# Performance work log

Measured on AMD Instinct MI355X. Metric: run time of the kernel, lower is better.

The kernel has to match this reference:

```python
import jax, jax.numpy as jnp
import numpy as np

BAG = 15          # bag_size
STEPS = 5
LAM = 1e-3        # anti_hebb_lambda
PS = 8            # patch_size
IM = 28           # image_size
DEN = IM - PS     # position normalization denominator (=20)
KEEP = 0.1        # 1 - recurrent_sparsity


def _ln(h, gamma, beta, eps=1e-5):
    mu = jnp.mean(h, axis=-1, keepdims=True)
    var = jnp.mean((h - mu) ** 2, axis=-1, keepdims=True)
    return (h - mu) * jax.lax.rsqrt(var + eps) * gamma + beta


def _patch(img, pos):
    # img: [IM, IM], pos: [2] int32 -> flattened PSxPS patch [PS*PS]
    return jax.lax.dynamic_slice(img, (pos[0], pos[1]), (PS, PS)).reshape(PS * PS)

_extract = jax.vmap(_patch)  # [B,IM,IM], [B,2] -> [B, PS*PS]


def setup_inputs() -> dict:
    key = jax.random.key(0)
    ks = jax.random.split(key, 8)
    B = 65536
    x = jax.random.normal(ks[0], (B, 1, IM, IM), jnp.float32)
    in_dim = PS * PS + 2
    Wi = jax.random.normal(ks[1], (BAG, in_dim), jnp.float32) * np.sqrt(2.0 / in_dim)
    bi = jnp.zeros((BAG,), jnp.float32)
    gamma = jnp.ones((BAG,), jnp.float32)
    beta = jnp.zeros((BAG,), jnp.float32)
    mask = (jax.random.uniform(ks[2], (BAG, BAG)) < KEEP).astype(jnp.float32)
    R = jax.random.normal(ks[3], (BAG, BAG), jnp.float32) * np.sqrt(2.0 / BAG) * mask
    rb = jnp.zeros((BAG,), jnp.float32)
    Wc = jax.random.normal(ks[4], (2, BAG), jnp.float32) * np.sqrt(2.0 / BAG)
    bc = jnp.zeros((2,), jnp.float32)
    Wo = jax.random.normal(ks[5], (10, BAG), jnp.float32) * np.sqrt(2.0 / BAG)
    bo = jnp.zeros((10,), jnp.float32)
    return dict(x=x, Wi=Wi, bi=bi, gamma=gamma, beta=beta, R=R, rb=rb,
                mask=mask, Wc=Wc, bc=bc, Wo=Wo, bo=bo)


def reference(x, Wi, bi, gamma, beta, R, rb, mask, Wc, bc, Wo, bo):
    B = x.shape[0]
    imgs = x[:, 0]  # [B, IM, IM]
    positions = jnp.full((B, 2), (IM - PS) // 2, dtype=jnp.int32)
    state = None
    logits = None
    for _ in range(STEPS):  # small fixed step count; state/positions recur
        flat = _extract(imgs, positions)                       # [B, 64]
        pos = positions.astype(x.dtype) / DEN * 2.0 - 1.0      # [B, 2]
        in_act = jnp.concatenate([flat, pos], axis=1) @ Wi.T + bi
        if state is None:
            state = _ln(jax.nn.relu(in_act), gamma, beta)
        else:
            coact = jnp.einsum('bi,bj->ij', state, state) / B  # [BAG, BAG]
            Reff = (R - LAM * coact) * mask
            state = _ln(jax.nn.relu(in_act + state @ Reff.T + rb), gamma, beta)
        logits = state @ Wo.T + bo                             # [B, 10]
        ctrl = jnp.tanh(state @ Wc.T + bc)                     # [B, 2]
        mag_r = jnp.abs(ctrl[:, 0])
        mag_c = jnp.abs(ctrl[:, 1])
        row_sel = mag_r >= mag_c
        row_move = jnp.where(row_sel, jnp.sign(ctrl[:, 0]).astype(jnp.int32), 0)
        col_move = jnp.where(row_sel, 0, jnp.sign(ctrl[:, 1]).astype(jnp.int32))
        positions = jnp.clip(positions + jnp.stack([row_move, col_move], axis=1), 0, IM - PS)
    return logits
```

## Files before the change

kernel.cpp:

```cpp
#include <hip/hip_runtime.h>
#include <math.h>

#define BAGN 15
#define PSZ 8
#define IMSZ 28
#define LAMF 0.001f

template<bool FIRST, bool LAST>
__global__ __launch_bounds__(256) void step_kernel(
    const float* __restrict__ x,
    const float* __restrict__ Wi, const float* __restrict__ bi,
    const float* __restrict__ gamma, const float* __restrict__ beta,
    const float* __restrict__ R, const float* __restrict__ rb,
    const float* __restrict__ mask,
    const float* __restrict__ Wc, const float* __restrict__ bc,
    const float* __restrict__ Wo, const float* __restrict__ bo,
    float* __restrict__ state_io, int* __restrict__ pos_io,
    const float* __restrict__ coact_in, float* __restrict__ coact_out,
    float* __restrict__ out, int B, float invB)
{
    __shared__ float sWi[15 * 72];
    __shared__ float sBi[15], sGa[15], sBe[15], sRb[15];
    __shared__ float sWc[30], sBc[2], sWo[150], sBo[10];
    __shared__ float sReff[225];
    __shared__ float sS[256 * 16];

    const int tid = threadIdx.x;

    for (int idx = tid; idx < 990; idx += 256) {
        int u = idx / 66, k = idx - u * 66;
        sWi[u * 72 + k] = Wi[idx];
    }
    if (tid < 15) {
        sBi[tid] = bi[tid]; sGa[tid] = gamma[tid];
        sBe[tid] = beta[tid]; sRb[tid] = rb[tid];
    }
    if (tid >= 32 && tid < 62) sWc[tid - 32] = Wc[tid - 32];
    if (tid >= 64 && tid < 66) sBc[tid - 64] = bc[tid - 64];
    if (LAST) {
        if (tid >= 96 && tid < 246) sWo[tid - 96] = Wo[tid - 96];
        if (tid >= 246 && tid < 256) sBo[tid - 246] = bo[tid - 246];
    }
    if (!FIRST) {
        if (tid < 225)
            sReff[tid] = (R[tid] - LAMF * (coact_in[tid] * invB)) * mask[tid];
    }
    __syncthreads();

    const int b = blockIdx.x * 256 + tid;

    int pr, pc;
    if (FIRST) { pr = 10; pc = 10; }
    else { pr = pos_io[b]; pc = pos_io[B + b]; }

    const float* img = x + (size_t)b * (IMSZ * IMSZ);
    float patch[64];
#pragma unroll
    for (int r = 0; r < 8; ++r) {
        const float* rowp = img + (pr + r) * IMSZ + pc;
#pragma unroll
        for (int c = 0; c < 8; ++c) patch[r * 8 + c] = rowp[c];
    }
    const float posr = ((float)pr / 20.0f) * 2.0f - 1.0f;
    const float posc = ((float)pc / 20.0f) * 2.0f - 1.0f;

    float sprev[15];
    if (!FIRST) {
#pragma unroll
        for (int j = 0; j < 15; ++j) sprev[j] = state_io[j * B + b];
    }

    float h[15];
#pragma unroll
    for (int u = 0; u < 15; ++u) {
        const float* w = sWi + u * 72;
        float a = 0.0f;
#pragma unroll
        for (int k = 0; k < 64; ++k) a = fmaf(patch[k], w[k], a);
        a = fmaf(posr, w[64], a);
        a = fmaf(posc, w[65], a);
        a += sBi[u];
        if (!FIRST) {
            float r2 = 0.0f;
#pragma unroll
            for (int j = 0; j < 15; ++j) r2 = fmaf(sprev[j], sReff[u * 15 + j], r2);
            a += r2 + sRb[u];
        }
        h[u] = a > 0.0f ? a : 0.0f;
    }

    float mu = 0.0f;
#pragma unroll
    for (int u = 0; u < 15; ++u) mu += h[u];
    mu *= (1.0f / 15.0f);
    float var = 0.0f;
#pragma unroll
    for (int u = 0; u < 15; ++u) { float d = h[u] - mu; var = fmaf(d, d, var); }
    var *= (1.0f / 15.0f);
    const float rs = 1.0f / sqrtf(var + 1e-5f);
    float s[15];
#pragma unroll
    for (int u = 0; u < 15; ++u) s[u] = (h[u] - mu) * rs * sGa[u] + sBe[u];

    if (LAST) {
#pragma unroll
        for (int o = 0; o < 10; ++o) {
            float a = 0.0f;
#pragma unroll
            for (int j = 0; j < 15; ++j) a = fmaf(s[j], sWo[o * 15 + j], a);
            out[(size_t)b * 10 + o] = a + sBo[o];
        }
    } else {
#pragma unroll
        for (int j = 0; j < 15; ++j) state_io[j * B + b] = s[j];

        float c0 = 0.0f, c1 = 0.0f;
#pragma unroll
        for (int j = 0; j < 15; ++j) {
            c0 = fmaf(s[j], sWc[j], c0);
            c1 = fmaf(s[j], sWc[15 + j], c1);
        }
        c0 = tanhf(c0 + sBc[0]);
        c1 = tanhf(c1 + sBc[1]);
        const float m0 = fabsf(c0), m1 = fabsf(c1);
        int rm, cm;
        if (m0 >= m1) { rm = (c0 > 0.0f) - (c0 < 0.0f); cm = 0; }
        else          { rm = 0; cm = (c1 > 0.0f) - (c1 < 0.0f); }
        pr += rm; pc += cm;
        pr = min(max(pr, 0), IMSZ - PSZ);
        pc = min(max(pc, 0), IMSZ - PSZ);
        pos_io[b] = pr;
        pos_io[B + b] = pc;

#pragma unroll
        for (int j = 0; j < 15; ++j) sS[tid * 16 + j] = s[j];
        __syncthreads();
        if (tid < 225) {
            int i = tid / 15, j = tid - i * 15;
            float acc = 0.0f;
#pragma unroll 8
            for (int bb = 0; bb < 256; ++bb)
                acc = fmaf(sS[bb * 16 + i], sS[bb * 16 + j], acc);
            atomicAdd(&coact_out[tid], acc);
        }
    }
}

extern "C" void kernel_launch(void* const* d_in, const int* in_sizes, int n_in,
                              void* d_out, int out_size, void* d_ws, size_t ws_size,
                              hipStream_t stream) {
    const float* x     = (const float*)d_in[0];
    const float* Wi    = (const float*)d_in[1];
    const float* bi    = (const float*)d_in[2];
    const float* gamma = (const float*)d_in[3];
    const float* beta  = (const float*)d_in[4];
    const float* R     = (const float*)d_in[5];
    const float* rb    = (const float*)d_in[6];
    const float* mask  = (const float*)d_in[7];
    const float* Wc    = (const float*)d_in[8];
    const float* bc    = (const float*)d_in[9];
    const float* Wo    = (const float*)d_in[10];
    const float* bo    = (const float*)d_in[11];
    float* out = (float*)d_out;

    const int B = in_sizes[0] / (IMSZ * IMSZ);
    const int grid = B / 256;
    const float invB = 1.0f / (float)B;

    float* wsf = (float*)d_ws;
    float* state = wsf;
    int* pos = (int*)(wsf + (size_t)B * 15);
    float* coact = wsf + (size_t)B * 15 + (size_t)B * 2;

    hipMemsetAsync(coact, 0, 4 * 256 * sizeof(float), stream);

    step_kernel<true, false><<<grid, 256, 0, stream>>>(
        x, Wi, bi, gamma, beta, R, rb, mask, Wc, bc, Wo, bo,
        state, pos, nullptr, coact, nullptr, B, invB);
    step_kernel<false, false><<<grid, 256, 0, stream>>>(
        x, Wi, bi, gamma, beta, R, rb, mask, Wc, bc, Wo, bo,
        state, pos, coact, coact + 256, nullptr, B, invB);
    step_kernel<false, false><<<grid, 256, 0, stream>>>(
        x, Wi, bi, gamma, beta, R, rb, mask, Wc, bc, Wo, bo,
        state, pos, coact + 256, coact + 512, nullptr, B, invB);
    step_kernel<false, false><<<grid, 256, 0, stream>>>(
        x, Wi, bi, gamma, beta, R, rb, mask, Wc, bc, Wo, bo,
        state, pos, coact + 512, coact + 768, nullptr, B, invB);
    step_kernel<false, true><<<grid, 256, 0, stream>>>(
        x, Wi, bi, gamma, beta, R, rb, mask, Wc, bc, Wo, bo,
        state, pos, coact + 768, nullptr, out, B, invB);
}
```

Baseline: 383.8 us.

## Fuse all recurrent steps into one cooperative kernel with grid-wide syncs

Replaces the five per-step launches with a single cooperative kernel that loops over the steps. Recurrent state and patch positions stay in registers instead of round-tripping through global workspace. A grid.sync after each step's coactivation reduction provides the global dependency. The coactivation accumulators are padded to a 16-float stride so concurrent atomics do not share cache lines. In exchange it pays for grid-wide barriers and requires all 256 blocks to be co-resident, which limits occupancy for hiding the latency of the patch gathers.

```diff
diff --git a/kernel.cpp b/kernel.cpp
--- a/kernel.cpp
+++ b/kernel.cpp
@@ -1,13 +1,14 @@
 #include <hip/hip_runtime.h>
+#include <hip/hip_cooperative_groups.h>
 #include <math.h>
 
-#define BAGN 15
+namespace cg = cooperative_groups;
+
+#define IMSZ 28
 #define PSZ 8
-#define IMSZ 28
 #define LAMF 0.001f
 
-template<bool FIRST, bool LAST>
-__global__ __launch_bounds__(256) void step_kernel(
+__global__ __launch_bounds__(256) void cyclic_fused(
     const float* __restrict__ x,
     const float* __restrict__ Wi, const float* __restrict__ bi,
     const float* __restrict__ gamma, const float* __restrict__ beta,
@@ -15,14 +16,15 @@
     const float* __restrict__ mask,
     const float* __restrict__ Wc, const float* __restrict__ bc,
     const float* __restrict__ Wo, const float* __restrict__ bo,
-    float* __restrict__ state_io, int* __restrict__ pos_io,
-    const float* __restrict__ coact_in, float* __restrict__ coact_out,
+    float* __restrict__ coact,
     float* __restrict__ out, int B, float invB)
 {
+    cg::grid_group grid = cg::this_grid();
+
     __shared__ float sWi[15 * 72];
-    __shared__ float sBi[15], sGa[15], sBe[15], sRb[15];
-    __shared__ float sWc[30], sBc[2], sWo[150], sBo[10];
-    __shared__ float sReff[225];
+    __shared__ float sBi[16], sGa[16], sBe[16], sRb[16];
+    __shared__ float sWc[32], sBc[2], sWo[160], sBo[16];
+    __shared__ float sR[240], sM[240], sReff[240];
     __shared__ float sS[256 * 16];
 
     const int tid = threadIdx.x;
@@ -31,117 +33,110 @@
         int u = idx / 66, k = idx - u * 66;
         sWi[u * 72 + k] = Wi[idx];
     }
+    if (tid < 225) { sR[tid] = R[tid]; sM[tid] = mask[tid]; }
     if (tid < 15) {
         sBi[tid] = bi[tid]; sGa[tid] = gamma[tid];
         sBe[tid] = beta[tid]; sRb[tid] = rb[tid];
     }
-    if (tid >= 32 && tid < 62) sWc[tid - 32] = Wc[tid - 32];
-    if (tid >= 64 && tid < 66) sBc[tid - 64] = bc[tid - 64];
-    if (LAST) {
-        if (tid >= 96 && tid < 246) sWo[tid - 96] = Wo[tid - 96];
-        if (tid >= 246 && tid < 256) sBo[tid - 246] = bo[tid - 246];
-    }
-    if (!FIRST) {
-        if (tid < 225)
-            sReff[tid] = (R[tid] - LAMF * (coact_in[tid] * invB)) * mask[tid];
-    }
+    if (tid < 30)  sWc[tid] = Wc[tid];
+    if (tid < 2)   sBc[tid] = bc[tid];
+    if (tid < 150) sWo[tid] = Wo[tid];
+    if (tid < 10)  sBo[tid] = bo[tid];
     __syncthreads();
 
     const int b = blockIdx.x * 256 + tid;
+    const float* img = x + (size_t)b * (IMSZ * IMSZ);
 
-    int pr, pc;
-    if (FIRST) { pr = 10; pc = 10; }
-    else { pr = pos_io[b]; pc = pos_io[B + b]; }
+    int pr = 10, pc = 10;
+    float st[15];
 
-    const float* img = x + (size_t)b * (IMSZ * IMSZ);
-    float patch[64];
+    for (int s = 0; s < 5; ++s) {
+        float patch[64];
 #pragma unroll
-    for (int r = 0; r < 8; ++r) {
-        const float* rowp = img + (pr + r) * IMSZ + pc;
+        for (int r = 0; r < 8; ++r) {
+            const float* rowp = img + (pr + r) * IMSZ + pc;
 #pragma unroll
-        for (int c = 0; c < 8; ++c) patch[r * 8 + c] = rowp[c];
-    }
-    const float posr = ((float)pr / 20.0f) * 2.0f - 1.0f;
-    const float posc = ((float)pc / 20.0f) * 2.0f - 1.0f;
+            for (int c = 0; c < 8; ++c) patch[r * 8 + c] = rowp[c];
+        }
+        const float posr = ((float)pr / 20.0f) * 2.0f - 1.0f;
+        const float posc = ((float)pc / 20.0f) * 2.0f - 1.0f;
 
-    float sprev[15];
-    if (!FIRST) {
+        float h[15];
 #pragma unroll
-        for (int j = 0; j < 15; ++j) sprev[j] = state_io[j * B + b];
-    }
-
-    float h[15];
-#pragma unroll
-    for (int u = 0; u < 15; ++u) {
-        const float* w = sWi + u * 72;
-        float a = 0.0f;
-#pragma unroll
-        for (int k = 0; k < 64; ++k) a = fmaf(patch[k], w[k], a);
-        a = fmaf(posr, w[64], a);
-        a = fmaf(posc, w[65], a);
-        a += sBi[u];
-        if (!FIRST) {
-            float r2 = 0.0f;
-#pragma unroll
-            for (int j = 0; j < 15; ++j) r2 = fmaf(sprev[j], sReff[u * 15 + j], r2);
-            a += r2 + sRb[u];
-        }
-        h[u] = a > 0.0f ? a : 0.0f;
-    }
-
-    float mu = 0.0f;
-#pragma unroll
-    for (int u = 0; u < 15; ++u) mu += h[u];
-    mu *= (1.0f / 15.0f);
-    float var = 0.0f;
-#pragma unroll
-    for (int u = 0; u < 15; ++u) { float d = h[u] - mu; var = fmaf(d, d, var); }
-    var *= (1.0f / 15.0f);
-    const float rs = 1.0f / sqrtf(var + 1e-5f);
-    float s[15];
-#pragma unroll
-    for (int u = 0; u < 15; ++u) s[u] = (h[u] - mu) * rs * sGa[u] + sBe[u];
-
-    if (LAST) {
-#pragma unroll
-        for (int o = 0; o < 10; ++o) {
+        for (int u = 0; u < 15; ++u) {
+            const float* w = sWi + u * 72;
             float a = 0.0f;
 #pragma unroll
-            for (int j = 0; j < 15; ++j) a = fmaf(s[j], sWo[o * 15 + j], a);
-            out[(size_t)b * 10 + o] = a + sBo[o];
+            for (int k = 0; k < 64; ++k) a = fmaf(patch[k], w[k], a);
+            a = fmaf(posr, w[64], a);
+            a = fmaf(posc, w[65], a);
+            a += sBi[u];
+            if (s > 0) {
+                float r2 = 0.0f;
+#pragma unroll
+                for (int j = 0; j < 15; ++j) r2 = fmaf(st[j], sReff[u * 15 + j], r2);
+                a += r2 + sRb[u];
+            }
+            h[u] = fmaxf(a, 0.0f);
         }
-    } else {
+
+        float mu = 0.0f;
 #pragma unroll
-        for (int j = 0; j < 15; ++j) state_io[j * B + b] = s[j];
+        for (int u = 0; u < 15; ++u) mu += h[u];
+        mu *= (1.0f / 15.0f);
+        float var = 0.0f;
+#pragma unroll
+        for (int u = 0; u < 15; ++u) { float d = h[u] - mu; var = fmaf(d, d, var); }
+        var *= (1.0f / 15.0f);
+        const float rs = 1.0f / sqrtf(var + 1e-5f);
+#pragma unroll
+        for (int u = 0; u < 15; ++u) st[u] = (h[u] - mu) * rs * sGa[u] + sBe[u];
 
-        float c0 = 0.0f, c1 = 0.0f;
+        if (s == 4) {
 #pragma unroll
-        for (int j = 0; j < 15; ++j) {
-            c0 = fmaf(s[j], sWc[j], c0);
-            c1 = fmaf(s[j], sWc[15 + j], c1);
-        }
-        c0 = tanhf(c0 + sBc[0]);
-        c1 = tanhf(c1 + sBc[1]);
-        const float m0 = fabsf(c0), m1 = fabsf(c1);
-        int rm, cm;
-        if (m0 >= m1) { rm = (c0 > 0.0f) - (c0 < 0.0f); cm = 0; }
-        else          { rm = 0; cm = (c1 > 0.0f) - (c1 < 0.0f); }
-        pr += rm; pc += cm;
-        pr = min(max(pr, 0), IMSZ - PSZ);
-        pc = min(max(pc, 0), IMSZ - PSZ);
-        pos_io[b] = pr;
-        pos_io[B + b] = pc;
+            for (int o = 0; o < 10; ++o) {
+                float a = 0.0f;
+#pragma unroll
+                for (int j = 0; j < 15; ++j) a = fmaf(st[j], sWo[o * 15 + j], a);
+                out[(size_t)b * 10 + o] = a + sBo[o];
+            }
+        } else {
+#pragma unroll
+            for (int j = 0; j < 15; ++j) sS[tid * 16 + j] = st[j];
 
+            float c0 = 0.0f, c1 = 0.0f;
 #pragma unroll
-        for (int j = 0; j < 15; ++j) sS[tid * 16 + j] = s[j];
-        __syncthreads();
-        if (tid < 225) {
-            int i = tid / 15, j = tid - i * 15;
-            float acc = 0.0f;
+            for (int j = 0; j < 15; ++j) {
+                c0 = fmaf(st[j], sWc[j], c0);
+                c1 = fmaf(st[j], sWc[15 + j], c1);
+            }
+            c0 = tanhf(c0 + sBc[0]);
+            c1 = tanhf(c1 + sBc[1]);
+            const float m0 = fabsf(c0), m1 = fabsf(c1);
+            int rm, cm;
+            if (m0 >= m1) { rm = (c0 > 0.0f) - (c0 < 0.0f); cm = 0; }
+            else          { rm = 0; cm = (c1 > 0.0f) - (c1 < 0.0f); }
+            pr = min(max(pr + rm, 0), IMSZ - PSZ);
+            pc = min(max(pc + cm, 0), IMSZ - PSZ);
+
+            __syncthreads();
+            if (tid < 225) {
+                int i = tid / 15, j = tid - i * 15;
+                float acc = 0.0f;
 #pragma unroll 8
-            for (int bb = 0; bb < 256; ++bb)
-                acc = fmaf(sS[bb * 16 + i], sS[bb * 16 + j], acc);
-            atomicAdd(&coact_out[tid], acc);
+                for (int bb = 0; bb < 256; ++bb)
+                    acc = fmaf(sS[bb * 16 + i], sS[bb * 16 + j], acc);
+                atomicAdd(&coact[(size_t)(s * 225 + tid) * 16], acc);
+            }
+
+            grid.sync();
+
+            if (tid < 225) {
+                float cv = __hip_atomic_load(&coact[(size_t)(s * 225 + tid) * 16],
+                                             __ATOMIC_ACQUIRE, __HIP_MEMORY_SCOPE_AGENT);
+                sReff[tid] = (sR[tid] - LAMF * (cv * invB)) * sM[tid];
+            }
+            __syncthreads();
         }
     }
 }
@@ -163,30 +158,17 @@
     const float* bo    = (const float*)d_in[11];
     float* out = (float*)d_out;
 
-    const int B = in_sizes[0] / (IMSZ * IMSZ);
-    const int grid = B / 256;
-    const float invB = 1.0f / (float)B;
+    int B = in_sizes[0] / (IMSZ * IMSZ);
+    float invB = 1.0f / (float)B;
+    float* coact = (float*)d_ws;
 
-    float* wsf = (float*)d_ws;
-    float* state = wsf;
-    int* pos = (int*)(wsf + (size_t)B * 15);
-    float* coact = wsf + (size_t)B * 15 + (size_t)B * 2;
+    hipMemsetAsync(coact, 0, (size_t)4 * 240 * 16 * sizeof(float), stream);
 
-    hipMemsetAsync(coact, 0, 4 * 256 * sizeof(float), stream);
+    void* args[] = { (void*)&x, (void*)&Wi, (void*)&bi, (void*)&gamma, (void*)&beta,
+                     (void*)&R, (void*)&rb, (void*)&mask, (void*)&Wc, (void*)&bc,
+                     (void*)&Wo, (void*)&bo, (void*)&coact, (void*)&out,
+                     (void*)&B, (void*)&invB };
 
-    step_kernel<true, false><<<grid, 256, 0, stream>>>(
-        x, Wi, bi, gamma, beta, R, rb, mask, Wc, bc, Wo, bo,
-        state, pos, nullptr, coact, nullptr, B, invB);
-    step_kernel<false, false><<<grid, 256, 0, stream>>>(
-        x, Wi, bi, gamma, beta, R, rb, mask, Wc, bc, Wo, bo,
-        state, pos, coact, coact + 256, nullptr, B, invB);
-    step_kernel<false, false><<<grid, 256, 0, stream>>>(
-        x, Wi, bi, gamma, beta, R, rb, mask, Wc, bc, Wo, bo,
-        state, pos, coact + 256, coact + 512, nullptr, B, invB);
-    step_kernel<false, false><<<grid, 256, 0, stream>>>(
-        x, Wi, bi, gamma, beta, R, rb, mask, Wc, bc, Wo, bo,
-        state, pos, coact + 512, coact + 768, nullptr, B, invB);
-    step_kernel<false, true><<<grid, 256, 0, stream>>>(
-        x, Wi, bi, gamma, beta, R, rb, mask, Wc, bc, Wo, bo,
-        state, pos, coact + 768, nullptr, out, B, invB);
+    hipLaunchCooperativeKernel((void*)cyclic_fused, dim3(B / 256), dim3(256),
+                               args, 0, stream);
 }
```

Result: slower. 534.3 us (+39.2%).

## Split each sample across 8 lanes with shuffle reduction and replicated coact atomics

Applied to the files above, without the earlier changes.

Each sample is now handled by 8 threads: each lane loads one patch row and computes partial dot products, which are combined with xor shuffles. Before, one thread gathered a whole 64-element patch with strided loads. State moves to a row-major stride-16 layout and positions are packed into one int. Coactivation partials are spread over 8 replicated accumulators to cut atomic contention, now that blocks hold 32 samples and there are 8x more of them. The cost is redundant per-lane layer-norm, control math and weight reloads in every block.

```diff
diff --git a/kernel.cpp b/kernel.cpp
--- a/kernel.cpp
+++ b/kernel.cpp
@@ -1,13 +1,14 @@
 #include <hip/hip_runtime.h>
 #include <math.h>
 
-#define BAGN 15
-#define PSZ 8
 #define IMSZ 28
+#define PSZ  8
 #define LAMF 0.001f
+#define NREP 8
+#define CSTRIDE 240
 
 template<bool FIRST, bool LAST>
-__global__ __launch_bounds__(256) void step_kernel(
+__global__ __launch_bounds__(256, 8) void step8(
     const float* __restrict__ x,
     const float* __restrict__ Wi, const float* __restrict__ bi,
     const float* __restrict__ gamma, const float* __restrict__ beta,
@@ -15,15 +16,15 @@
     const float* __restrict__ mask,
     const float* __restrict__ Wc, const float* __restrict__ bc,
     const float* __restrict__ Wo, const float* __restrict__ bo,
-    float* __restrict__ state_io, int* __restrict__ pos_io,
+    float* __restrict__ state, int* __restrict__ pos,
     const float* __restrict__ coact_in, float* __restrict__ coact_out,
     float* __restrict__ out, int B, float invB)
 {
     __shared__ float sWi[15 * 72];
-    __shared__ float sBi[15], sGa[15], sBe[15], sRb[15];
-    __shared__ float sWc[30], sBc[2], sWo[150], sBo[10];
-    __shared__ float sReff[225];
-    __shared__ float sS[256 * 16];
+    __shared__ float sBi[16], sGa[16], sBe[16], sRb[16];
+    __shared__ float sWc[32], sBc[2], sWo[160], sBo[16];
+    __shared__ float sReff[240];
+    __shared__ float sS[32 * 16];
 
     const int tid = threadIdx.x;
 
@@ -39,54 +40,69 @@
     if (tid >= 64 && tid < 66) sBc[tid - 64] = bc[tid - 64];
     if (LAST) {
         if (tid >= 96 && tid < 246) sWo[tid - 96] = Wo[tid - 96];
-        if (tid >= 246 && tid < 256) sBo[tid - 246] = bo[tid - 246];
+        if (tid >= 246) sBo[tid - 246] = bo[tid - 246];
     }
     if (!FIRST) {
-        if (tid < 225)
-            sReff[tid] = (R[tid] - LAMF * (coact_in[tid] * invB)) * mask[tid];
+        if (tid < 225) {
+            float cv = 0.0f;
+#pragma unroll
+            for (int r = 0; r < NREP; ++r) cv += coact_in[r * CSTRIDE + tid];
+            sReff[tid] = (R[tid] - LAMF * (cv * invB)) * mask[tid];
+        } else if (tid < 240) {
+            sReff[tid] = 0.0f;
+        }
     }
     __syncthreads();
 
-    const int b = blockIdx.x * 256 + tid;
+    const int sib = tid >> 3;
+    const int row = tid & 7;
+    const int b = blockIdx.x * 32 + sib;
 
     int pr, pc;
     if (FIRST) { pr = 10; pc = 10; }
-    else { pr = pos_io[b]; pc = pos_io[B + b]; }
-
-    const float* img = x + (size_t)b * (IMSZ * IMSZ);
-    float patch[64];
-#pragma unroll
-    for (int r = 0; r < 8; ++r) {
-        const float* rowp = img + (pr + r) * IMSZ + pc;
-#pragma unroll
-        for (int c = 0; c < 8; ++c) patch[r * 8 + c] = rowp[c];
-    }
+    else { int p = pos[b]; pr = p >> 8; pc = p & 255; }
+
+    const float* rowp = x + (size_t)b * (IMSZ * IMSZ) + (pr + row) * IMSZ + pc;
+    float patch[8];
+#pragma unroll
+    for (int c = 0; c < 8; ++c) patch[c] = rowp[c];
+
     const float posr = ((float)pr / 20.0f) * 2.0f - 1.0f;
     const float posc = ((float)pc / 20.0f) * 2.0f - 1.0f;
 
-    float sprev[15];
+    float sj0 = 0.0f, sj1 = 0.0f;
     if (!FIRST) {
-#pragma unroll
-        for (int j = 0; j < 15; ++j) sprev[j] = state_io[j * B + b];
+        sj0 = state[b * 16 + row];
+        sj1 = (row < 7) ? state[b * 16 + 8 + row] : 0.0f;
     }
 
     float h[15];
 #pragma unroll
     for (int u = 0; u < 15; ++u) {
-        const float* w = sWi + u * 72;
+        const float* w = sWi + u * 72 + row * 8;
         float a = 0.0f;
 #pragma unroll
-        for (int k = 0; k < 64; ++k) a = fmaf(patch[k], w[k], a);
-        a = fmaf(posr, w[64], a);
-        a = fmaf(posc, w[65], a);
-        a += sBi[u];
+        for (int c = 0; c < 8; ++c) a = fmaf(patch[c], w[c], a);
         if (!FIRST) {
-            float r2 = 0.0f;
-#pragma unroll
-            for (int j = 0; j < 15; ++j) r2 = fmaf(sprev[j], sReff[u * 15 + j], r2);
-            a += r2 + sRb[u];
-        }
-        h[u] = a > 0.0f ? a : 0.0f;
+            a = fmaf(sj0, sReff[u * 15 + row], a);
+            a = fmaf(sj1, sReff[u * 15 + 8 + row], a);
+        }
+        if (row == 0) {
+            a = fmaf(posr, sWi[u * 72 + 64], a);
+            a = fmaf(posc, sWi[u * 72 + 65], a);
+            a += sBi[u];
+            if (!FIRST) a += sRb[u];
+        }
+        h[u] = a;
+    }
+
+#pragma unroll
+    for (int u = 0; u < 15; ++u) {
+        float v = h[u];
+        v += __shfl_xor(v, 1);
+        v += __shfl_xor(v, 2);
+        v += __shfl_xor(v, 4);
+        h[u] = fmaxf(v, 0.0f);
     }
 
     float mu = 0.0f;
@@ -98,27 +114,30 @@
     for (int u = 0; u < 15; ++u) { float d = h[u] - mu; var = fmaf(d, d, var); }
     var *= (1.0f / 15.0f);
     const float rs = 1.0f / sqrtf(var + 1e-5f);
-    float s[15];
-#pragma unroll
-    for (int u = 0; u < 15; ++u) s[u] = (h[u] - mu) * rs * sGa[u] + sBe[u];
+    float st[15];
+#pragma unroll
+    for (int u = 0; u < 15; ++u) st[u] = (h[u] - mu) * rs * sGa[u] + sBe[u];
 
     if (LAST) {
 #pragma unroll
-        for (int o = 0; o < 10; ++o) {
-            float a = 0.0f;
-#pragma unroll
-            for (int j = 0; j < 15; ++j) a = fmaf(s[j], sWo[o * 15 + j], a);
-            out[(size_t)b * 10 + o] = a + sBo[o];
+        for (int rep = 0; rep < 2; ++rep) {
+            int o = rep * 8 + row;
+            if (o < 10) {
+                float a = 0.0f;
+#pragma unroll
+                for (int j = 0; j < 15; ++j) a = fmaf(st[j], sWo[o * 15 + j], a);
+                out[(size_t)b * 10 + o] = a + sBo[o];
+            }
         }
     } else {
-#pragma unroll
-        for (int j = 0; j < 15; ++j) state_io[j * B + b] = s[j];
+        state[b * 16 + row] = st[row];
+        if (row < 7) state[b * 16 + 8 + row] = st[8 + row];
 
         float c0 = 0.0f, c1 = 0.0f;
 #pragma unroll
         for (int j = 0; j < 15; ++j) {
-            c0 = fmaf(s[j], sWc[j], c0);
-            c1 = fmaf(s[j], sWc[15 + j], c1);
+            c0 = fmaf(st[j], sWc[j], c0);
+            c1 = fmaf(st[j], sWc[15 + j], c1);
         }
         c0 = tanhf(c0 + sBc[0]);
         c1 = tanhf(c1 + sBc[1]);
@@ -126,22 +145,20 @@
         int rm, cm;
         if (m0 >= m1) { rm = (c0 > 0.0f) - (c0 < 0.0f); cm = 0; }
         else          { rm = 0; cm = (c1 > 0.0f) - (c1 < 0.0f); }
-        pr += rm; pc += cm;
-        pr = min(max(pr, 0), IMSZ - PSZ);
-        pc = min(max(pc, 0), IMSZ - PSZ);
-        pos_io[b] = pr;
-        pos_io[B + b] = pc;
-
-#pragma unroll
-        for (int j = 0; j < 15; ++j) sS[tid * 16 + j] = s[j];
+        pr = min(max(pr + rm, 0), IMSZ - PSZ);
+        pc = min(max(pc + cm, 0), IMSZ - PSZ);
+        if (row == 0) pos[b] = (pr << 8) | pc;
+
+        sS[sib * 16 + row] = st[row];
+        if (row < 7) sS[sib * 16 + 8 + row] = st[8 + row];
         __syncthreads();
         if (tid < 225) {
             int i = tid / 15, j = tid - i * 15;
             float acc = 0.0f;
-#pragma unroll 8
-            for (int bb = 0; bb < 256; ++bb)
+#pragma unroll
+            for (int bb = 0; bb < 32; ++bb)
                 acc = fmaf(sS[bb * 16 + i], sS[bb * 16 + j], acc);
-            atomicAdd(&coact_out[tid], acc);
+            atomicAdd(&coact_out[(blockIdx.x & (NREP - 1)) * CSTRIDE + tid], acc);
         }
     }
 }
@@ -164,29 +181,29 @@
     float* out = (float*)d_out;
 
     const int B = in_sizes[0] / (IMSZ * IMSZ);
-    const int grid = B / 256;
     const float invB = 1.0f / (float)B;
+    const int grid = B / 32;
 
     float* wsf = (float*)d_ws;
     float* state = wsf;
-    int* pos = (int*)(wsf + (size_t)B * 15);
-    float* coact = wsf + (size_t)B * 15 + (size_t)B * 2;
-
-    hipMemsetAsync(coact, 0, 4 * 256 * sizeof(float), stream);
-
-    step_kernel<true, false><<<grid, 256, 0, stream>>>(
-        x, Wi, bi, gamma, beta, R, rb, mask, Wc, bc, Wo, bo,
-        state, pos, nullptr, coact, nullptr, B, invB);
-    step_kernel<false, false><<<grid, 256, 0, stream>>>(
-        x, Wi, bi, gamma, beta, R, rb, mask, Wc, bc, Wo, bo,
-        state, pos, coact, coact + 256, nullptr, B, invB);
-    step_kernel<false, false><<<grid, 256, 0, stream>>>(
-        x, Wi, bi, gamma, beta, R, rb, mask, Wc, bc, Wo, bo,
-        state, pos, coact + 256, coact + 512, nullptr, B, invB);
-    step_kernel<false, false><<<grid, 256, 0, stream>>>(
-        x, Wi, bi, gamma, beta, R, rb, mask, Wc, bc, Wo, bo,
-        state, pos, coact + 512, coact + 768, nullptr, B, invB);
-    step_kernel<false, true><<<grid, 256, 0, stream>>>(
-        x, Wi, bi, gamma, beta, R, rb, mask, Wc, bc, Wo, bo,
-        state, pos, coact + 768, nullptr, out, B, invB);
+    int* pos = (int*)(wsf + (size_t)B * 16);
+    float* coact = wsf + (size_t)B * 16 + (size_t)B;
+
+    hipMemsetAsync(coact, 0, (size_t)4 * NREP * CSTRIDE * sizeof(float), stream);
+
+    step8<true, false><<<grid, 256, 0, stream>>>(
+        x, Wi, bi, gamma, beta, R, rb, mask, Wc, bc, Wo, bo,
+        state, pos, nullptr, coact + 0 * NREP * CSTRIDE, nullptr, B, invB);
+    step8<false, false><<<grid, 256, 0, stream>>>(
+        x, Wi, bi, gamma, beta, R, rb, mask, Wc, bc, Wo, bo,
+        state, pos, coact + 0 * NREP * CSTRIDE, coact + 1 * NREP * CSTRIDE, nullptr, B, invB);
+    step8<false, false><<<grid, 256, 0, stream>>>(
+        x, Wi, bi, gamma, beta, R, rb, mask, Wc, bc, Wo, bo,
+        state, pos, coact + 1 * NREP * CSTRIDE, coact + 2 * NREP * CSTRIDE, nullptr, B, invB);
+    step8<false, false><<<grid, 256, 0, stream>>>(
+        x, Wi, bi, gamma, beta, R, rb, mask, Wc, bc, Wo, bo,
+        state, pos, coact + 2 * NREP * CSTRIDE, coact + 3 * NREP * CSTRIDE, nullptr, B, invB);
+    step8<false, true><<<grid, 256, 0, stream>>>(
+        x, Wi, bi, gamma, beta, R, rb, mask, Wc, bc, Wo, bo,
+        state, pos, coact + 3 * NREP * CSTRIDE, nullptr, out, B, invB);
 }
```

Result: faster. 353.3 us (-7.9%).

## Vectorize patch loads, read weights directly, symmetric coact with replicated atomics

Applied to the files above, without the earlier changes.

Patch rows are now loaded as aligned float4 triples and shifted with selects, replacing scalar gathers. Weights are read directly from global memory (uniform scalar loads) instead of being staged in shared memory, which removes the prologue barrier. The coactivation is accumulated only for the 120 upper-triangle pairs into 8 replicated accumulators selected by block index, reducing atomic contention. Positions are packed into one int, and launch bounds request a single block per SM. The risk is extra per-thread work: every thread rebuilds Reff from global coact sums (8 replicas times 225 entries), which may cost more than it saves.

```diff
diff --git a/kernel.cpp b/kernel.cpp
--- a/kernel.cpp
+++ b/kernel.cpp
@@ -1,13 +1,15 @@
 #include <hip/hip_runtime.h>
 #include <math.h>
 
-#define BAGN 15
-#define PSZ 8
 #define IMSZ 28
+#define PSZ  8
 #define LAMF 0.001f
+#define NREP 8
+#define NPAIR 120
+#define CSTR 128
 
 template<bool FIRST, bool LAST>
-__global__ __launch_bounds__(256) void step_kernel(
+__global__ __launch_bounds__(256, 1) void step_spt(
     const float* __restrict__ x,
     const float* __restrict__ Wi, const float* __restrict__ bi,
     const float* __restrict__ gamma, const float* __restrict__ beta,
@@ -15,133 +17,149 @@
     const float* __restrict__ mask,
     const float* __restrict__ Wc, const float* __restrict__ bc,
     const float* __restrict__ Wo, const float* __restrict__ bo,
-    float* __restrict__ state_io, int* __restrict__ pos_io,
+    float* __restrict__ state, int* __restrict__ pos,
     const float* __restrict__ coact_in, float* __restrict__ coact_out,
-    float* __restrict__ out, int B, float invB)
+    float* __restrict__ out, int B, float lamB)
 {
-    __shared__ float sWi[15 * 72];
-    __shared__ float sBi[15], sGa[15], sBe[15], sRb[15];
-    __shared__ float sWc[30], sBc[2], sWo[150], sBo[10];
-    __shared__ float sReff[225];
     __shared__ float sS[256 * 16];
 
     const int tid = threadIdx.x;
-
-    for (int idx = tid; idx < 990; idx += 256) {
-        int u = idx / 66, k = idx - u * 66;
-        sWi[u * 72 + k] = Wi[idx];
-    }
-    if (tid < 15) {
-        sBi[tid] = bi[tid]; sGa[tid] = gamma[tid];
-        sBe[tid] = beta[tid]; sRb[tid] = rb[tid];
-    }
-    if (tid >= 32 && tid < 62) sWc[tid - 32] = Wc[tid - 32];
-    if (tid >= 64 && tid < 66) sBc[tid - 64] = bc[tid - 64];
-    if (LAST) {
-        if (tid >= 96 && tid < 246) sWo[tid - 96] = Wo[tid - 96];
-        if (tid >= 246 && tid < 256) sBo[tid - 246] = bo[tid - 246];
-    }
-    if (!FIRST) {
-        if (tid < 225)
-            sReff[tid] = (R[tid] - LAMF * (coact_in[tid] * invB)) * mask[tid];
-    }
-    __syncthreads();
-
     const int b = blockIdx.x * 256 + tid;
+    const float* img = x + (size_t)b * (IMSZ * IMSZ);
 
     int pr, pc;
     if (FIRST) { pr = 10; pc = 10; }
-    else { pr = pos_io[b]; pc = pos_io[B + b]; }
-
-    const float* img = x + (size_t)b * (IMSZ * IMSZ);
+    else { int p = pos[b]; pr = p >> 8; pc = p & 255; }
+
     float patch[64];
-#pragma unroll
-    for (int r = 0; r < 8; ++r) {
-        const float* rowp = img + (pr + r) * IMSZ + pc;
-#pragma unroll
-        for (int c = 0; c < 8; ++c) patch[r * 8 + c] = rowp[c];
-    }
+    {
+        const int base = pr * IMSZ + pc;
+        const int a0 = base & ~3;
+        if (FIRST) {
+#pragma unroll
+            for (int r = 0; r < 8; ++r) {
+                const float4* q = (const float4*)(img + a0 + r * IMSZ);
+                float4 q0 = q[0], q1 = q[1], q2 = q[2];
+                patch[r * 8 + 0] = q0.z; patch[r * 8 + 1] = q0.w;
+                patch[r * 8 + 2] = q1.x; patch[r * 8 + 3] = q1.y;
+                patch[r * 8 + 4] = q1.z; patch[r * 8 + 5] = q1.w;
+                patch[r * 8 + 6] = q2.x; patch[r * 8 + 7] = q2.y;
+            }
+        } else {
+            const int d = base & 3;
+            const bool s2 = (d & 2) != 0, s1 = (d & 1) != 0;
+#pragma unroll
+            for (int r = 0; r < 8; ++r) {
+                const float4* q = (const float4*)(img + a0 + r * IMSZ);
+                float4 q0 = q[0], q1 = q[1], q2 = q[2];
+                const float f[12] = { q0.x, q0.y, q0.z, q0.w,
+                                      q1.x, q1.y, q1.z, q1.w,
+                                      q2.x, q2.y, q2.z, q2.w };
+                float t[9];
+#pragma unroll
+                for (int c = 0; c < 9; ++c) t[c] = s2 ? f[c + 2] : f[c];
+#pragma unroll
+                for (int c = 0; c < 8; ++c) patch[r * 8 + c] = s1 ? t[c + 1] : t[c];
+            }
+        }
+    }
+
     const float posr = ((float)pr / 20.0f) * 2.0f - 1.0f;
     const float posc = ((float)pc / 20.0f) * 2.0f - 1.0f;
 
-    float sprev[15];
-    if (!FIRST) {
-#pragma unroll
-        for (int j = 0; j < 15; ++j) sprev[j] = state_io[j * B + b];
-    }
-
     float h[15];
 #pragma unroll
     for (int u = 0; u < 15; ++u) {
-        const float* w = sWi + u * 72;
+        const float* w = Wi + u * 66;
         float a = 0.0f;
 #pragma unroll
         for (int k = 0; k < 64; ++k) a = fmaf(patch[k], w[k], a);
         a = fmaf(posr, w[64], a);
         a = fmaf(posc, w[65], a);
-        a += sBi[u];
-        if (!FIRST) {
-            float r2 = 0.0f;
-#pragma unroll
-            for (int j = 0; j < 15; ++j) r2 = fmaf(sprev[j], sReff[u * 15 + j], r2);
-            a += r2 + sRb[u];
-        }
-        h[u] = a > 0.0f ? a : 0.0f;
-    }
-
+        h[u] = a + bi[u];
+    }
+
+    if (!FIRST) {
+        float sprev[15];
+#pragma unroll
+        for (int j = 0; j < 15; ++j) sprev[j] = state[(size_t)j * B + b];
+#pragma unroll
+        for (int j = 0; j < 15; ++j) {
+            const float sj = sprev[j];
+#pragma unroll
+            for (int u = 0; u < 15; ++u) {
+                const int i0 = u < j ? u : j;
+                const int j0 = u < j ? j : u;
+                const int sid = i0 * 15 + j0 - (i0 * (i0 + 1)) / 2;
+                float cs = 0.0f;
+#pragma unroll
+                for (int rr = 0; rr < NREP; ++rr) cs += coact_in[rr * CSTR + sid];
+                const float reff = (R[u * 15 + j] - lamB * cs) * mask[u * 15 + j];
+                h[u] = fmaf(sj, reff, h[u]);
+            }
+        }
+#pragma unroll
+        for (int u = 0; u < 15; ++u) h[u] += rb[u];
+    }
+
+#pragma unroll
+    for (int u = 0; u < 15; ++u) h[u] = fmaxf(h[u], 0.0f);
     float mu = 0.0f;
 #pragma unroll
     for (int u = 0; u < 15; ++u) mu += h[u];
     mu *= (1.0f / 15.0f);
     float var = 0.0f;
 #pragma unroll
-    for (int u = 0; u < 15; ++u) { float d = h[u] - mu; var = fmaf(d, d, var); }
+    for (int u = 0; u < 15; ++u) { float dd = h[u] - mu; var = fmaf(dd, dd, var); }
     var *= (1.0f / 15.0f);
     const float rs = 1.0f / sqrtf(var + 1e-5f);
-    float s[15];
-#pragma unroll
-    for (int u = 0; u < 15; ++u) s[u] = (h[u] - mu) * rs * sGa[u] + sBe[u];
+    float st[15];
+#pragma unroll
+    for (int u = 0; u < 15; ++u) st[u] = (h[u] - mu) * rs * gamma[u] + beta[u];
 
     if (LAST) {
 #pragma unroll
         for (int o = 0; o < 10; ++o) {
             float a = 0.0f;
 #pragma unroll
-            for (int j = 0; j < 15; ++j) a = fmaf(s[j], sWo[o * 15 + j], a);
-            out[(size_t)b * 10 + o] = a + sBo[o];
+            for (int j = 0; j < 15; ++j) a = fmaf(st[j], Wo[o * 15 + j], a);
+            out[(size_t)b * 10 + o] = a + bo[o];
         }
     } else {
 #pragma unroll
-        for (int j = 0; j < 15; ++j) state_io[j * B + b] = s[j];
+        for (int j = 0; j < 15; ++j) state[(size_t)j * B + b] = st[j];
 
         float c0 = 0.0f, c1 = 0.0f;
 #pragma unroll
         for (int j = 0; j < 15; ++j) {
-            c0 = fmaf(s[j], sWc[j], c0);
-            c1 = fmaf(s[j], sWc[15 + j], c1);
-        }
-        c0 = tanhf(c0 + sBc[0]);
-        c1 = tanhf(c1 + sBc[1]);
+            c0 = fmaf(st[j], Wc[j], c0);
+            c1 = fmaf(st[j], Wc[15 + j], c1);
+        }
+        c0 = tanhf(c0 + bc[0]);
+        c1 = tanhf(c1 + bc[1]);
         const float m0 = fabsf(c0), m1 = fabsf(c1);
         int rm, cm;
         if (m0 >= m1) { rm = (c0 > 0.0f) - (c0 < 0.0f); cm = 0; }
         else          { rm = 0; cm = (c1 > 0.0f) - (c1 < 0.0f); }
-        pr += rm; pc += cm;
-        pr = min(max(pr, 0), IMSZ - PSZ);
-        pc = min(max(pc, 0), IMSZ - PSZ);
-        pos_io[b] = pr;
-        pos_io[B + b] = pc;
-
-#pragma unroll
-        for (int j = 0; j < 15; ++j) sS[tid * 16 + j] = s[j];
+        pr = min(max(pr + rm, 0), IMSZ - PSZ);
+        pc = min(max(pc + cm, 0), IMSZ - PSZ);
+        pos[b] = (pr << 8) | pc;
+
+        float4* sv = (float4*)&sS[tid * 16];
+        sv[0] = make_float4(st[0], st[1], st[2], st[3]);
+        sv[1] = make_float4(st[4], st[5], st[6], st[7]);
+        sv[2] = make_float4(st[8], st[9], st[10], st[11]);
+        sv[3] = make_float4(st[12], st[13], st[14], 0.0f);
         __syncthreads();
-        if (tid < 225) {
-            int i = tid / 15, j = tid - i * 15;
+        if (tid < NPAIR) {
+            int i = 0, p = tid;
+            while (p >= 15 - i) { p -= 15 - i; ++i; }
+            const int j = i + p;
             float acc = 0.0f;
 #pragma unroll 8
             for (int bb = 0; bb < 256; ++bb)
                 acc = fmaf(sS[bb * 16 + i], sS[bb * 16 + j], acc);
-            atomicAdd(&coact_out[tid], acc);
+            atomicAdd(&coact_out[(blockIdx.x & (NREP - 1)) * CSTR + tid], acc);
         }
     }
 }
@@ -164,29 +182,29 @@
     float* out = (float*)d_out;
 
     const int B = in_sizes[0] / (IMSZ * IMSZ);
+    const float lamB = LAMF / (float)B;
     const int grid = B / 256;
-    const float invB = 1.0f / (float)B;
 
     float* wsf = (float*)d_ws;
     float* state = wsf;
-    int* pos = (int*)(wsf + (size_t)B * 15);
-    float* coact = wsf + (size_t)B * 15 + (size_t)B * 2;
-
-    hipMemsetAsync(coact, 0, 4 * 256 * sizeof(float), stream);
-
-    step_kernel<true, false><<<grid, 256, 0, stream>>>(
-        x, Wi, bi, gamma, beta, R, rb, mask, Wc, bc, Wo, bo,
-        state, pos, nullptr, coact, nullptr, B, invB);
-    step_kernel<false, false><<<grid, 256, 0, stream>>>(
-        x, Wi, bi, gamma, beta, R, rb, mask, Wc, bc, Wo, bo,
-        state, pos, coact, coact + 256, nullptr, B, invB);
-    step_kernel<false, false><<<grid, 256, 0, stream>>>(
-        x, Wi, bi, gamma, beta, R, rb, mask, Wc, bc, Wo, bo,
-        state, pos, coact + 256, coact + 512, nullptr, B, invB);
-    step_kernel<false, false><<<grid, 256, 0, stream>>>(
-        x, Wi, bi, gamma, beta, R, rb, mask, Wc, bc, Wo, bo,
-        state, pos, coact + 512, coact + 768, nullptr, B, invB);
-    step_kernel<false, true><<<grid, 256, 0, stream>>>(
-        x, Wi, bi, gamma, beta, R, rb, mask, Wc, bc, Wo, bo,
-        state, pos, coact + 768, nullptr, out, B, invB);
+    int* pos = (int*)(wsf + (size_t)15 * B);
+    float* coact = wsf + (size_t)15 * B + (size_t)B;
+
+    hipMemsetAsync(coact, 0, (size_t)4 * NREP * CSTR * sizeof(float), stream);
+
+    step_spt<true, false><<<grid, 256, 0, stream>>>(
+        x, Wi, bi, gamma, beta, R, rb, mask, Wc, bc, Wo, bo,
+        state, pos, nullptr, coact + 0 * NREP * CSTR, nullptr, B, lamB);
+    step_spt<false, false><<<grid, 256, 0, stream>>>(
+        x, Wi, bi, gamma, beta, R, rb, mask, Wc, bc, Wo, bo,
+        state, pos, coact + 0 * NREP * CSTR, coact + 1 * NREP * CSTR, nullptr, B, lamB);
+    step_spt<false, false><<<grid, 256, 0, stream>>>(
+        x, Wi, bi, gamma, beta, R, rb, mask, Wc, bc, Wo, bo,
+        state, pos, coact + 1 * NREP * CSTR, coact + 2 * NREP * CSTR, nullptr, B, lamB);
+    step_spt<false, false><<<grid, 256, 0, stream>>>(
+        x, Wi, bi, gamma, beta, R, rb, mask, Wc, bc, Wo, bo,
+        state, pos, coact + 2 * NREP * CSTR, coact + 3 * NREP * CSTR, nullptr, B, lamB);
+    step_spt<false, true><<<grid, 256, 0, stream>>>(
+        x, Wi, bi, gamma, beta, R, rb, mask, Wc, bc, Wo, bo,
+        state, pos, coact + 3 * NREP * CSTR, nullptr, out, B, lamB);
 }
```

After: 636.1 us. +65.7%, slower.
